# Optimization experiments

Hardware: AMD Instinct MI355X
Metric: run time of the kernel (lower is better)

Reference implementation:

```python
import jax, jax.numpy as jnp
import numpy as np

B, S, D, H = 2, 2048, 1024, 16
DK = D // H  # 64
THETA = 10000.0


def _rope_tables(seq_len, d_k, theta):
    pos = jnp.arange(seq_len, dtype=jnp.float32)  # [S]
    dim = jnp.arange(0, d_k, 2, dtype=jnp.float32)  # [DK/2]
    inv_freq = 1.0 / theta ** (dim / d_k)
    angle = pos[:, None] * inv_freq[None, :]  # [S, DK/2]
    angle = jnp.repeat(angle, 2, axis=-1)  # repeat_interleave -> [S, DK]
    return jnp.cos(angle), jnp.sin(angle)


def _apply_rope(x, cos, sin):
    # x: [..., S, DK]; interleaved pair rotation
    x1 = x[..., ::2]
    x2 = x[..., 1::2]
    x_perm = jnp.stack([-x2, x1], axis=-1).reshape(x.shape)
    return x * cos + x_perm * sin


def setup_inputs() -> dict:
    key = jax.random.key(0)
    ks = jax.random.split(key, 5)
    std = np.sqrt(2.0 / (D + D)).astype(np.float32)
    return {
        "x": jax.random.normal(ks[0], (B, S, D), dtype=jnp.float32),
        "Wq": jax.random.normal(ks[1], (D, D), dtype=jnp.float32) * std,
        "Wk": jax.random.normal(ks[2], (D, D), dtype=jnp.float32) * std,
        "Wv": jax.random.normal(ks[3], (D, D), dtype=jnp.float32) * std,
        "Wo": jax.random.normal(ks[4], (D, D), dtype=jnp.float32) * std,
    }


def reference(x, Wq, Wk, Wv, Wo):
    seq_len = x.shape[-2]
    # projections: weight is [d_out, d_in], applied as x @ W^T
    def split_heads(t):
        return t.reshape(*t.shape[:-1], H, DK).swapaxes(-3, -2)  # [B, H, S, DK]

    Q = split_heads(jnp.einsum('bsd,od->bso', x, Wq))
    K = split_heads(jnp.einsum('bsd,od->bso', x, Wk))
    V = split_heads(jnp.einsum('bsd,od->bso', x, Wv))

    cos, sin = _rope_tables(seq_len, DK, THETA)  # [S, DK]
    Q = _apply_rope(Q, cos, sin)
    K = _apply_rope(K, cos, sin)

    scale = 1.0 / np.sqrt(DK).astype(np.float32)
    logits = jnp.einsum('bhnd,bhmd->bhnm', Q, K) * scale  # [B, H, S, S]
    causal = jnp.tril(jnp.ones((seq_len, seq_len), dtype=bool))
    logits = jnp.where(causal, logits, -jnp.inf)
    probs = jax.nn.softmax(logits, axis=-1)
    attn = jnp.einsum('bhnm,bhmd->bhnd', probs, V)  # [B, H, S, DK]
    attn = attn.swapaxes(-3, -2).reshape(*x.shape[:-1], D)  # [B, S, D]
    return jnp.einsum('bsd,od->bso', attn, Wo)
```

## Files before the change

kernel.cpp:

```cpp
#include <hip/hip_runtime.h>
#include <hip/hip_bf16.h>
#include <cstdint>
#include <cstddef>

#define BB 2
#define SS 2048
#define DD 1024
#define HH 16
#define DKK 64
#define MM (BB*SS)

typedef __bf16 bf16x8 __attribute__((ext_vector_type(8)));
typedef float  f32x4  __attribute__((ext_vector_type(4)));

__device__ __forceinline__ unsigned short f2bf(float f) {
    unsigned u = __float_as_uint(f);
    u += 0x7FFF + ((u >> 16) & 1);
    return (unsigned short)(u >> 16);
}

#if __has_builtin(__builtin_amdgcn_cvt_pk_bf16_f32)
typedef __bf16 bf16v2 __attribute__((ext_vector_type(2)));
__device__ __forceinline__ unsigned pk_bf16(float a, float b) {
    bf16v2 v = __builtin_amdgcn_cvt_pk_bf16_f32(a, b);
    return __builtin_bit_cast(unsigned, v);
}
#else
__device__ __forceinline__ unsigned pk_bf16(float a, float b) {
    return (unsigned)f2bf(a) | ((unsigned)f2bf(b) << 16);
}
#endif

__device__ __forceinline__ void gld_lds16(const void* g, void* l) {
    __builtin_amdgcn_global_load_lds(
        (const __attribute__((address_space(1))) unsigned int*)g,
        (__attribute__((address_space(3))) unsigned int*)l, 16, 0, 0);
}

#define WAIT_VM8() __builtin_amdgcn_s_waitcnt(0x0F78)
#define WAIT_VM4() __builtin_amdgcn_s_waitcnt(0x0F74)
#define WAIT_VM3() __builtin_amdgcn_s_waitcnt(0x0F73)
#define WAIT_VM0() __builtin_amdgcn_s_waitcnt(0x0F70)
#define BARRIER()  __builtin_amdgcn_s_barrier()

__global__ __launch_bounds__(256) void cast_all(const float* __restrict__ x,
                                                const float* __restrict__ wq,
                                                const float* __restrict__ wk,
                                                const float* __restrict__ wv,
                                                const float* __restrict__ wo,
                                                unsigned short* __restrict__ xb,
                                                unsigned short* __restrict__ wb) {
    int i = (blockIdx.x * 256 + threadIdx.x) * 4;
    const float* src;
    unsigned short* dst;
    if (i < MM * DD) { src = x + i; dst = xb + i; }
    else {
        int e = i - MM * DD;
        int r = e >> 20;
        const float* s0 = (r == 0) ? wq : (r == 1) ? wk : (r == 2) ? wv : wo;
        src = s0 + (e & ((1 << 20) - 1));
        dst = wb + e;
    }
    float4 v = *reinterpret_cast<const float4*>(src);
    ushort4 o;
    o.x = f2bf(v.x); o.y = f2bf(v.y); o.z = f2bf(v.z); o.w = f2bf(v.w);
    *reinterpret_cast<ushort4*>(dst) = o;
}

__global__ __launch_bounds__(256, 3) void gemm_qkv(const unsigned short* __restrict__ A,
                                                   const unsigned short* __restrict__ W,
                                                   unsigned short* __restrict__ Qo,
                                                   unsigned short* __restrict__ Ko,
                                                   unsigned short* __restrict__ Vto) {
    __shared__ __align__(16) unsigned short A0[128 * 32], W0[128 * 32];
    __shared__ __align__(16) unsigned short A1[128 * 32], W1[128 * 32];
    const int tid  = threadIdx.x;
    const int wave = tid >> 6, lane = tid & 63;
    const int quad = lane >> 4, l16 = lane & 15;
    const int wm = wave >> 1, wn = wave & 1;
    const int m0 = blockIdx.y * 128, n0 = blockIdx.x * 128;
    const int sw3 = l16 & 3;

    f32x4 acc[4][4];
    for (int i = 0; i < 4; i++)
        for (int j = 0; j < 4; j++) acc[i][j] = f32x4{0.f, 0.f, 0.f, 0.f};

    auto stage = [&](int k0, unsigned short* As, unsigned short* Ws) {
        for (int c = tid; c < 512; c += 256) {
            int row = c >> 2, g = c & 3;
            int gc = ((g ^ (row & 3)) << 3);
            gld_lds16(A + (size_t)(m0 + row) * DD + k0 + gc, As + c * 8);
            gld_lds16(W + (size_t)(n0 + row) * DD + k0 + gc, Ws + c * 8);
        }
    };
    auto compute = [&](const unsigned short* As, const unsigned short* Ws) {
        bf16x8 af[4], bfb[4];
        for (int i = 0; i < 4; i++)
            af[i] = *reinterpret_cast<const bf16x8*>(As + (wm * 64 + i * 16 + l16) * 32 + ((quad ^ sw3) << 3));
        for (int j = 0; j < 4; j++)
            bfb[j] = *reinterpret_cast<const bf16x8*>(Ws + (wn * 64 + j * 16 + l16) * 32 + ((quad ^ sw3) << 3));
        for (int i = 0; i < 4; i++)
            for (int j = 0; j < 4; j++)
                acc[i][j] = __builtin_amdgcn_mfma_f32_16x16x32_bf16(af[i], bfb[j], acc[i][j], 0, 0, 0);
    };

    stage(0, A0, W0);
    int k0 = 0;
    while (true) {
        BARRIER();
        if (k0 + 32 < DD) { stage(k0 + 32, A1, W1); WAIT_VM4(); } else WAIT_VM0();
        BARRIER();
        compute(A0, W0);
        k0 += 32; if (k0 >= DD) break;

        BARRIER();
        if (k0 + 32 < DD) { stage(k0 + 32, A0, W0); WAIT_VM4(); } else WAIT_VM0();
        BARRIER();
        compute(A1, W1);
        k0 += 32; if (k0 >= DD) break;
    }

    const int region = n0 >> 10;
    const float L2T_OVER_DK = 13.287712379549449f / 64.0f;
    if (region < 2) {
        unsigned short* Co = region ? Ko : Qo;
        for (int i = 0; i < 4; i++) {
            int mrow = m0 + wm * 64 + i * 16 + quad * 4;
            int b = mrow >> 11, s0 = mrow & 2047;
            for (int j = 0; j < 4; j++) {
                int nc = (n0 + wn * 64 + j * 16 + l16) & 1023;
                int h = nc >> 6, dk = nc & 63;
                float inv_freq = exp2f(-(float)(dk & ~1) * L2T_OVER_DK);
                for (int r = 0; r < 4; r++) {
                    float v = acc[i][j][r];
                    float partner = __shfl_xor(v, 1, 64);
                    float sn, cs;
                    __sincosf((float)(s0 + r) * inv_freq, &sn, &cs);
                    float outv = v * cs + ((dk & 1) ? partner : -partner) * sn;
                    Co[((size_t)(b * HH + h) * SS + (s0 + r)) * DKK + dk] = f2bf(outv);
                }
            }
        }
    } else {
        __syncthreads();
        unsigned short* T = A0 + wave * 1024;
        const int dkl = lane >> 2, s4 = (lane & 3) * 4;
        for (int i = 0; i < 4; i++) {
            int ms0 = m0 + wm * 64 + i * 16;
            for (int j = 0; j < 4; j++) {
                int nc0 = n0 + wn * 64 + j * 16;
                for (int r = 0; r < 4; r++)
                    T[(quad * 4 + r) * 17 + l16] = f2bf(acc[i][j][r]);
                ushort4 o;
                o.x = T[(s4 + 0) * 17 + dkl];
                o.y = T[(s4 + 1) * 17 + dkl];
                o.z = T[(s4 + 2) * 17 + dkl];
                o.w = T[(s4 + 3) * 17 + dkl];
                int nc = (nc0 + dkl) & 1023;
                int h = nc >> 6, dk = nc & 63;
                int m = ms0 + s4;
                int b = m >> 11, s = m & 2047;
                *reinterpret_cast<ushort4*>(Vto + ((size_t)((b * HH + h) * DKK + dk)) * SS + s) = o;
            }
        }
    }
}

__global__ __launch_bounds__(256, 3) void gemm_out(const unsigned short* __restrict__ A,
                                                   const unsigned short* __restrict__ W,
                                                   float* __restrict__ C) {
    __shared__ __align__(16) unsigned short A0[64 * 32], W0[128 * 32];
    __shared__ __align__(16) unsigned short A1[64 * 32], W1[128 * 32];
    const int tid  = threadIdx.x;
    const int wave = tid >> 6, lane = tid & 63;
    const int quad = lane >> 4, l16 = lane & 15;
    const int wm = wave >> 1, wn = wave & 1;
    const int m0 = blockIdx.y * 64, n0 = blockIdx.x * 128;
    const int sw3 = l16 & 3;

    f32x4 acc[2][4];
    for (int i = 0; i < 2; i++)
        for (int j = 0; j < 4; j++) acc[i][j] = f32x4{0.f, 0.f, 0.f, 0.f};

    auto stage = [&](int k0, unsigned short* As, unsigned short* Ws) {
        {
            int row = tid >> 2, g = tid & 3;
            int gc = ((g ^ (row & 3)) << 3);
            gld_lds16(A + (size_t)(m0 + row) * DD + k0 + gc, As + tid * 8);
        }
        for (int c = tid; c < 512; c += 256) {
            int row = c >> 2, g = c & 3;
            int gc = ((g ^ (row & 3)) << 3);
            gld_lds16(W + (size_t)(n0 + row) * DD + k0 + gc, Ws + c * 8);
        }
    };
    auto compute = [&](const unsigned short* As, const unsigned short* Ws) {
        bf16x8 af[2], bfb[4];
        for (int i = 0; i < 2; i++)
            af[i] = *reinterpret_cast<const bf16x8*>(As + (wm * 32 + i * 16 + l16) * 32 + ((quad ^ sw3) << 3));
        for (int j = 0; j < 4; j++)
            bfb[j] = *reinterpret_cast<const bf16x8*>(Ws + (wn * 64 + j * 16 + l16) * 32 + ((quad ^ sw3) << 3));
        for (int i = 0; i < 2; i++)
            for (int j = 0; j < 4; j++)
                acc[i][j] = __builtin_amdgcn_mfma_f32_16x16x32_bf16(af[i], bfb[j], acc[i][j], 0, 0, 0);
    };

    stage(0, A0, W0);
    int k0 = 0;
    while (true) {
        BARRIER();
        if (k0 + 32 < DD) { stage(k0 + 32, A1, W1); WAIT_VM3(); } else WAIT_VM0();
        BARRIER();
        compute(A0, W0);
        k0 += 32; if (k0 >= DD) break;

        BARRIER();
        if (k0 + 32 < DD) { stage(k0 + 32, A0, W0); WAIT_VM3(); } else WAIT_VM0();
        BARRIER();
        compute(A1, W1);
        k0 += 32; if (k0 >= DD) break;
    }

    for (int i = 0; i < 2; i++) {
        int mrow = m0 + wm * 32 + i * 16 + quad * 4;
        for (int j = 0; j < 4; j++) {
            int ncol = n0 + wn * 64 + j * 16 + l16;
            for (int r = 0; r < 4; r++)
                C[(size_t)(mrow + r) * DD + ncol] = acc[i][j][r];
        }
    }
}

__global__ __launch_bounds__(256) void attn_kernel(const unsigned short* __restrict__ Qb,
                                                   const unsigned short* __restrict__ Kb,
                                                   const unsigned short* __restrict__ Vtb,
                                                   unsigned short* __restrict__ attn) {
    __shared__ unsigned short K0s[128 * 64], V0s[64 * 128];
    __shared__ unsigned short K1s[128 * 64], V1s[64 * 128];
    __shared__ unsigned short Ps[4][16 * 72];

    const int tid  = threadIdx.x;
    const int wave = tid >> 6, lane = tid & 63;
    const int quad = lane >> 4, l16 = lane & 15;
    const int t  = blockIdx.x;
    const int bh = blockIdx.y;
    const int swK = l16 & 7;
    const int qlo = t * 64, qhi = (31 - t) * 64;
    const int nIter = 32 - t;
    const int nStage = (nIter + 1) >> 1;

    const unsigned short* Qg = Qb  + (size_t)bh * SS * DKK;
    const unsigned short* Kg = Kb  + (size_t)bh * SS * DKK;
    const unsigned short* Vg = Vtb + (size_t)bh * DKK * SS;

    bf16x8 qL0 = *reinterpret_cast<const bf16x8*>(Qg + (size_t)(qlo + wave * 16 + l16) * DKK + quad * 8);
    bf16x8 qL1 = *reinterpret_cast<const bf16x8*>(Qg + (size_t)(qlo + wave * 16 + l16) * DKK + 32 + quad * 8);
    bf16x8 qH0 = *reinterpret_cast<const bf16x8*>(Qg + (size_t)(qhi + wave * 16 + l16) * DKK + quad * 8);
    bf16x8 qH1 = *reinterpret_cast<const bf16x8*>(Qg + (size_t)(qhi + wave * 16 + l16) * DKK + 32 + quad * 8);

    bf16x8 vone;
    for (int tt = 0; tt < 8; tt++) vone[tt] = (__bf16)1.0f;

    f32x4 aoL[4], aoH[4], alL, alH;
    for (int j = 0; j < 4; j++) { aoL[j] = f32x4{0.f,0.f,0.f,0.f}; aoH[j] = f32x4{0.f,0.f,0.f,0.f}; }
    alL = f32x4{0.f,0.f,0.f,0.f}; alH = f32x4{0.f,0.f,0.f,0.f};

    auto stage = [&](int s2, unsigned short* Kd, unsigned short* Vd) {
        const int kv0 = s2 * 128;
        for (int c = tid; c < 1024; c += 256) {
            int rowK = c >> 3, gK = c & 7;
            gld_lds16(Kg + (size_t)(kv0 + rowK) * DKK + ((gK ^ (rowK & 7)) << 3), Kd + c * 8);
            int rowV = c >> 4, gV = c & 15;
            gld_lds16(Vg + (size_t)rowV * SS + kv0 + ((gV ^ (rowV & 15)) << 3), Vd + c * 8);
        }
    };

    const float C1 = 0.18033688011112042f;
    const float NB = -11.541560327111707f;

    auto do_tile = [&](const unsigned short* Kd, const unsigned short* Vd, int sub,
                       bf16x8 q0f, bf16x8 q1f, bool diag,
                       f32x4* ao, f32x4& al) {
        f32x4 sc[4];
        for (int j = 0; j < 4; j++) {
            const unsigned short* kr = Kd + (sub * 64 + j * 16 + l16) * 64;
            bf16x8 kf0 = *reinterpret_cast<const bf16x8*>(kr + ((quad ^ swK) << 3));
            bf16x8 kf1 = *reinterpret_cast<const bf16x8*>(kr + (((4 + quad) ^ swK) << 3));
            f32x4 s = f32x4{0.f, 0.f, 0.f, 0.f};
            s = __builtin_amdgcn_mfma_f32_16x16x32_bf16(q0f, kf0, s, 0, 0, 0);
            s = __builtin_amdgcn_mfma_f32_16x16x32_bf16(q1f, kf1, s, 0, 0, 0);
            sc[j] = s;
        }
        if (diag) {
            for (int j = 0; j < 4; j++) {
                int lcol = j * 16 + l16;
                for (int r = 0; r < 4; r++) {
                    int lrow = wave * 16 + quad * 4 + r;
                    if (lcol > lrow) sc[j][r] = -1e30f;
                }
            }
        }
        for (int j = 0; j < 4; j++)
            for (int r = 0; r < 4; r++)
                sc[j][r] = exp2f(fmaf(sc[j][r], C1, NB));

        unsigned short* Pw = Ps[wave];
        for (int r = 0; r < 4; r++) {
            unsigned pA = pk_bf16(sc[0][r], sc[1][r]);
            unsigned pB = pk_bf16(sc[2][r], sc[3][r]);
            int ro = (quad * 4 + r) * 72;
            Pw[ro + l16]      = (unsigned short)pA;
            Pw[ro + 16 + l16] = (unsigned short)(pA >> 16);
            Pw[ro + 32 + l16] = (unsigned short)pB;
            Pw[ro + 48 + l16] = (unsigned short)(pB >> 16);
        }

        for (int ko = 0; ko < 64; ko += 32) {
            bf16x8 pf = *reinterpret_cast<const bf16x8*>(Pw + l16 * 72 + ko + quad * 8);
            al = __builtin_amdgcn_mfma_f32_16x16x32_bf16(pf, vone, al, 0, 0, 0);
            int gg = sub * 8 + (ko >> 3) + quad;
            for (int j = 0; j < 4; j++) {
                bf16x8 vf = *reinterpret_cast<const bf16x8*>(Vd + (j * 16 + l16) * 128 + ((gg ^ l16) << 3));
                ao[j] = __builtin_amdgcn_mfma_f32_16x16x32_bf16(pf, vf, ao[j], 0, 0, 0);
            }
        }
    };

    auto process = [&](const unsigned short* Kd, const unsigned short* Vd, int s2) {
        for (int sub = 0; sub < 2; sub++) {
            int idx = 2 * s2 + sub;
            if (idx >= nIter) break;
            do_tile(Kd, Vd, sub, qH0, qH1, idx == nIter - 1, aoH, alH);
            if (idx <= t) do_tile(Kd, Vd, sub, qL0, qL1, idx == t, aoL, alL);
        }
    };

    stage(0, K0s, V0s);
    int s2 = 0;
    while (true) {
        BARRIER();
        if (s2 + 1 < nStage) { stage(s2 + 1, K1s, V1s); WAIT_VM8(); } else WAIT_VM0();
        BARRIER();
        process(K0s, V0s, s2);
        if (++s2 >= nStage) break;

        BARRIER();
        if (s2 + 1 < nStage) { stage(s2 + 1, K0s, V0s); WAIT_VM8(); } else WAIT_VM0();
        BARRIER();
        process(K1s, V1s, s2);
        if (++s2 >= nStage) break;
    }

    const int b = bh >> 4, h = bh & 15;
    for (int r = 0; r < 4; r++) {
        float invL = __builtin_amdgcn_rcpf(alL[r]);
        float invH = __builtin_amdgcn_rcpf(alH[r]);
        int srL = qlo + wave * 16 + quad * 4 + r;
        int srH = qhi + wave * 16 + quad * 4 + r;
        for (int j = 0; j < 4; j++) {
            attn[((size_t)(b * SS + srL)) * DD + h * DKK + j * 16 + l16] = f2bf(aoL[j][r] * invL);
            attn[((size_t)(b * SS + srH)) * DD + h * DKK + j * 16 + l16] = f2bf(aoH[j][r] * invH);
        }
    }
}

extern "C" void kernel_launch(void* const* d_in, const int* in_sizes, int n_in,
                              void* d_out, int out_size, void* d_ws, size_t ws_size,
                              hipStream_t stream) {
    const float* x  = (const float*)d_in[0];
    const float* Wq = (const float*)d_in[1];
    const float* Wk = (const float*)d_in[2];
    const float* Wv = (const float*)d_in[3];
    const float* Wo = (const float*)d_in[4];

    char* ws = (char*)d_ws;
    const size_t MB = 1u << 20;
    unsigned short* xb    = (unsigned short*)(ws);
    unsigned short* wb    = (unsigned short*)(ws + 8  * MB);
    unsigned short* Qbuf  = (unsigned short*)(ws + 16 * MB);
    unsigned short* Kbuf  = (unsigned short*)(ws + 24 * MB);
    unsigned short* Vtbuf = (unsigned short*)(ws + 32 * MB);
    unsigned short* attnb = xb;

    cast_all<<<8192, 256, 0, stream>>>(x, Wq, Wk, Wv, Wo, xb, wb);

    gemm_qkv<<<dim3(24, 32), 256, 0, stream>>>(xb, wb, Qbuf, Kbuf, Vtbuf);

    attn_kernel<<<dim3(16, BB * HH), 256, 0, stream>>>(Qbuf, Kbuf, Vtbuf, attnb);

    gemm_out<<<dim3(8, 64), 256, 0, stream>>>(attnb, wb + 3 * 1024 * 1024, (float*)d_out);
}
```

Baseline: 182.8 us.

## Replace paired causal q-tiles with one tile per block, XCD-aware scheduling

```diff
diff --git a/kernel.cpp b/kernel.cpp
--- a/kernel.cpp
+++ b/kernel.cpp
@@ -231,64 +231,63 @@
     }
 }
 
-__global__ __launch_bounds__(256) void attn_kernel(const unsigned short* __restrict__ Qb,
-                                                   const unsigned short* __restrict__ Kb,
-                                                   const unsigned short* __restrict__ Vtb,
-                                                   unsigned short* __restrict__ attn) {
-    __shared__ unsigned short K0s[128 * 64], V0s[64 * 128];
-    __shared__ unsigned short K1s[128 * 64], V1s[64 * 128];
+__global__ __launch_bounds__(256, 3) void attn_kernel(const unsigned short* __restrict__ Qb,
+                                                      const unsigned short* __restrict__ Kb,
+                                                      const unsigned short* __restrict__ Vtb,
+                                                      unsigned short* __restrict__ attn) {
+    __shared__ unsigned short K0s[64 * 64], V0s[64 * 64];
+    __shared__ unsigned short K1s[64 * 64], V1s[64 * 64];
     __shared__ unsigned short Ps[4][16 * 72];
 
     const int tid  = threadIdx.x;
     const int wave = tid >> 6, lane = tid & 63;
     const int quad = lane >> 4, l16 = lane & 15;
-    const int t  = blockIdx.x;
-    const int bh = blockIdx.y;
+
+    const int lin = blockIdx.x;
+    const int xcd = lin & 7, idx = lin >> 3;
+    const int bh  = xcd * 4 + (idx & 3);
+    const int tau = 31 - (idx >> 2);
+    const int nST = tau + 1;
+
     const int swK = l16 & 7;
-    const int qlo = t * 64, qhi = (31 - t) * 64;
-    const int nIter = 32 - t;
-    const int nStage = (nIter + 1) >> 1;
+    const int q0r = tau * 64;
 
     const unsigned short* Qg = Qb  + (size_t)bh * SS * DKK;
     const unsigned short* Kg = Kb  + (size_t)bh * SS * DKK;
     const unsigned short* Vg = Vtb + (size_t)bh * DKK * SS;
 
-    bf16x8 qL0 = *reinterpret_cast<const bf16x8*>(Qg + (size_t)(qlo + wave * 16 + l16) * DKK + quad * 8);
-    bf16x8 qL1 = *reinterpret_cast<const bf16x8*>(Qg + (size_t)(qlo + wave * 16 + l16) * DKK + 32 + quad * 8);
-    bf16x8 qH0 = *reinterpret_cast<const bf16x8*>(Qg + (size_t)(qhi + wave * 16 + l16) * DKK + quad * 8);
-    bf16x8 qH1 = *reinterpret_cast<const bf16x8*>(Qg + (size_t)(qhi + wave * 16 + l16) * DKK + 32 + quad * 8);
+    bf16x8 q0 = *reinterpret_cast<const bf16x8*>(Qg + (size_t)(q0r + wave * 16 + l16) * DKK + quad * 8);
+    bf16x8 q1 = *reinterpret_cast<const bf16x8*>(Qg + (size_t)(q0r + wave * 16 + l16) * DKK + 32 + quad * 8);
 
     bf16x8 vone;
     for (int tt = 0; tt < 8; tt++) vone[tt] = (__bf16)1.0f;
 
-    f32x4 aoL[4], aoH[4], alL, alH;
-    for (int j = 0; j < 4; j++) { aoL[j] = f32x4{0.f,0.f,0.f,0.f}; aoH[j] = f32x4{0.f,0.f,0.f,0.f}; }
-    alL = f32x4{0.f,0.f,0.f,0.f}; alH = f32x4{0.f,0.f,0.f,0.f};
-
-    auto stage = [&](int s2, unsigned short* Kd, unsigned short* Vd) {
-        const int kv0 = s2 * 128;
-        for (int c = tid; c < 1024; c += 256) {
+    f32x4 ao[4], al;
+    for (int j = 0; j < 4; j++) ao[j] = f32x4{0.f,0.f,0.f,0.f};
+    al = f32x4{0.f,0.f,0.f,0.f};
+
+    auto stage = [&](int s, unsigned short* Kd, unsigned short* Vd) {
+        const int kv0 = s * 64;
+        for (int c = tid; c < 512; c += 256) {
             int rowK = c >> 3, gK = c & 7;
             gld_lds16(Kg + (size_t)(kv0 + rowK) * DKK + ((gK ^ (rowK & 7)) << 3), Kd + c * 8);
-            int rowV = c >> 4, gV = c & 15;
-            gld_lds16(Vg + (size_t)rowV * SS + kv0 + ((gV ^ (rowV & 15)) << 3), Vd + c * 8);
+            int rowV = c >> 3, gV = c & 7;
+            gld_lds16(Vg + (size_t)rowV * SS + kv0 + ((gV ^ (rowV & 7)) << 3), Vd + c * 8);
         }
     };
 
     const float C1 = 0.18033688011112042f;
     const float NB = -11.541560327111707f;
 
-    auto do_tile = [&](const unsigned short* Kd, const unsigned short* Vd, int sub,
-                       bf16x8 q0f, bf16x8 q1f, bool diag,
-                       f32x4* ao, f32x4& al) {
+    auto do_tile = [&](const unsigned short* Kd, const unsigned short* Vd, bool diag) {
         f32x4 sc[4];
         for (int j = 0; j < 4; j++) {
-            const unsigned short* kr = Kd + (sub * 64 + j * 16 + l16) * 64;
+            const unsigned short* kr = Kd + (j * 16 + l16) * 64;
             bf16x8 kf0 = *reinterpret_cast<const bf16x8*>(kr + ((quad ^ swK) << 3));
             bf16x8 kf1 = *reinterpret_cast<const bf16x8*>(kr + (((4 + quad) ^ swK) << 3));
             f32x4 s = f32x4{0.f, 0.f, 0.f, 0.f};
-            s = __builtin_amdgcn_mfma_f32_16x16x32_bf16(q0f, kf0, s, 0, 0, 0);
-            s = __builtin_amdgcn_mfma_f32_16x16x32_bf16(q1f, kf1, s, 0, 0, 0);
+            s = __builtin_amdgcn_mfma_f32_16x16x32_bf16(q0, kf0, s, 0, 0, 0);
+            s = __builtin_amdgcn_mfma_f32_16x16x32_bf16(q1, kf1, s, 0, 0, 0);
             sc[j] = s;
         }
         if (diag) {
@@ -318,49 +317,36 @@
         for (int ko = 0; ko < 64; ko += 32) {
             bf16x8 pf = *reinterpret_cast<const bf16x8*>(Pw + l16 * 72 + ko + quad * 8);
             al = __builtin_amdgcn_mfma_f32_16x16x32_bf16(pf, vone, al, 0, 0, 0);
-            int gg = sub * 8 + (ko >> 3) + quad;
+            int gg = (ko >> 3) + quad;
             for (int j = 0; j < 4; j++) {
-                bf16x8 vf = *reinterpret_cast<const bf16x8*>(Vd + (j * 16 + l16) * 128 + ((gg ^ l16) << 3));
+                bf16x8 vf = *reinterpret_cast<const bf16x8*>(Vd + (j * 16 + l16) * 64 + ((gg ^ (l16 & 7)) << 3));
                 ao[j] = __builtin_amdgcn_mfma_f32_16x16x32_bf16(pf, vf, ao[j], 0, 0, 0);
             }
         }
     };
 
-    auto process = [&](const unsigned short* Kd, const unsigned short* Vd, int s2) {
-        for (int sub = 0; sub < 2; sub++) {
-            int idx = 2 * s2 + sub;
-            if (idx >= nIter) break;
-            do_tile(Kd, Vd, sub, qH0, qH1, idx == nIter - 1, aoH, alH);
-            if (idx <= t) do_tile(Kd, Vd, sub, qL0, qL1, idx == t, aoL, alL);
-        }
-    };
-
     stage(0, K0s, V0s);
-    int s2 = 0;
+    int s = 0;
     while (true) {
         BARRIER();
-        if (s2 + 1 < nStage) { stage(s2 + 1, K1s, V1s); WAIT_VM8(); } else WAIT_VM0();
-        BARRIER();
-        process(K0s, V0s, s2);
-        if (++s2 >= nStage) break;
-
-        BARRIER();
-        if (s2 + 1 < nStage) { stage(s2 + 1, K0s, V0s); WAIT_VM8(); } else WAIT_VM0();
-        BARRIER();
-        process(K1s, V1s, s2);
-        if (++s2 >= nStage) break;
+        if (s + 1 < nST) { stage(s + 1, K1s, V1s); WAIT_VM4(); } else WAIT_VM0();
+        BARRIER();
+        do_tile(K0s, V0s, s == tau);
+        if (++s >= nST) break;
+
+        BARRIER();
+        if (s + 1 < nST) { stage(s + 1, K0s, V0s); WAIT_VM4(); } else WAIT_VM0();
+        BARRIER();
+        do_tile(K1s, V1s, s == tau);
+        if (++s >= nST) break;
     }
 
     const int b = bh >> 4, h = bh & 15;
     for (int r = 0; r < 4; r++) {
-        float invL = __builtin_amdgcn_rcpf(alL[r]);
-        float invH = __builtin_amdgcn_rcpf(alH[r]);
-        int srL = qlo + wave * 16 + quad * 4 + r;
-        int srH = qhi + wave * 16 + quad * 4 + r;
-        for (int j = 0; j < 4; j++) {
-            attn[((size_t)(b * SS + srL)) * DD + h * DKK + j * 16 + l16] = f2bf(aoL[j][r] * invL);
-            attn[((size_t)(b * SS + srH)) * DD + h * DKK + j * 16 + l16] = f2bf(aoH[j][r] * invH);
-        }
+        float invL = __builtin_amdgcn_rcpf(al[r]);
+        int sr = q0r + wave * 16 + quad * 4 + r;
+        for (int j = 0; j < 4; j++)
+            attn[((size_t)(b * SS + sr)) * DD + h * DKK + j * 16 + l16] = f2bf(ao[j][r] * invL);
     }
 }
 
@@ -386,7 +372,7 @@
 
     gemm_qkv<<<dim3(24, 32), 256, 0, stream>>>(xb, wb, Qbuf, Kbuf, Vtbuf);
 
-    attn_kernel<<<dim3(16, BB * HH), 256, 0, stream>>>(Qbuf, Kbuf, Vtbuf, attnb);
+    attn_kernel<<<dim3(1024), 256, 0, stream>>>(Qbuf, Kbuf, Vtbuf, attnb);
 
     gemm_out<<<dim3(8, 64), 256, 0, stream>>>(attnb, wb + 3 * 1024 * 1024, (float*)d_out);
 }
```

New measurement: 178.4 us. 2.4% less time.
